# Performance work log

Hardware: AMD Instinct MI355X
Metric: run time of the kernel (lower is better)

## Reference

```python
import jax, jax.numpy as jnp
import numpy as np

EPS = 1e-08

def setup_inputs() -> dict:
    key = jax.random.key(0)
    k1, k2, k3, k4 = jax.random.split(key, 4)
    b, n, in_c, out_c, style_dim = 8, 4096, 512, 512, 512
    x = jax.random.normal(k1, (b, n, in_c), dtype=jnp.float32)
    style = jax.random.normal(k2, (b, style_dim), dtype=jnp.float32)
    # kaiming-ish scaled weights
    weight = jax.random.normal(k3, (1, in_c, out_c), dtype=jnp.float32) * np.float32(np.sqrt(2.0 / (1 + 0.2**2) / in_c))
    mod_w = jax.random.normal(k4, (in_c, style_dim), dtype=jnp.float32) * np.float32(np.sqrt(2.0 / (1 + 0.2**2) / style_dim))
    mod_b = jnp.zeros((in_c,), dtype=jnp.float32)
    return {"x": x, "style": style, "weight": weight, "mod_w": mod_w, "mod_b": mod_b}

def reference(x, style, weight, mod_w, mod_b):
    # style fc: (b, style_dim) -> (b, in_c)
    s = style @ mod_w.T + mod_b                      # (b, in)
    # modulate: broadcast base weight (1, in, out) by (s + 1)
    w = weight * (s[:, :, None] + 1.0)               # (b, in, out)
    # demodulate: rsqrt of sum of squares over in dim
    demod = jax.lax.rsqrt(jnp.sum(w * w, axis=1) + EPS)  # (b, out)
    w = w * demod[:, None, :]                        # (b, in, out)
    # batched matmul: (b, n, in) @ (b, in, out) -> (b, n, out)
    out = jnp.einsum('bni,bio->bno', x, w)
    return out
```

## Files before the change

kernel.cpp:

```cpp
#include <hip/hip_runtime.h>
#include <hip/hip_bf16.h>

typedef __bf16 bf16x4 __attribute__((ext_vector_type(4)));
typedef __bf16 bf16x8 __attribute__((ext_vector_type(8)));
typedef float f32x4 __attribute__((ext_vector_type(4)));

#define B_    8
#define NTOK  4096
#define CIN   512
#define COUT  512
#define SDIM  512
#define EPSF  1e-8f

__global__ __launch_bounds__(256) void k_stylefc(
    const float* __restrict__ style, const float* __restrict__ mod_w,
    const float* __restrict__ mod_b, float* __restrict__ m_out) {
  int gw   = (blockIdx.x * 256 + threadIdx.x) >> 6;
  int lane = threadIdx.x & 63;
  int b = gw >> 9;
  int i = gw & 511;
  const float* srow = style + (size_t)b * SDIM;
  const float* wrow = mod_w + (size_t)i * SDIM;
  float acc = 0.f;
#pragma unroll
  for (int k = 0; k < SDIM; k += 64) acc += srow[k + lane] * wrow[k + lane];
#pragma unroll
  for (int off = 32; off; off >>= 1) acc += __shfl_xor(acc, off, 64);
  if (lane == 0) m_out[b * CIN + i] = acc + mod_b[i] + 1.0f;
}

__global__ __launch_bounds__(256) void k_wprep(
    const float* __restrict__ weight, const float* __restrict__ m_buf,
    __bf16* __restrict__ wT, float* __restrict__ demod) {
  int o = blockIdx.x;
  int tid = threadIdx.x;
  int wid = tid >> 6, lane = tid & 63;
  float acc[B_] = {0.f, 0.f, 0.f, 0.f, 0.f, 0.f, 0.f, 0.f};
#pragma unroll
  for (int rep = 0; rep < 2; ++rep) {
    int i = tid + rep * 256;
    float w = weight[(size_t)i * COUT + o];
    wT[(size_t)o * CIN + i] = (__bf16)w;
#pragma unroll
    for (int b = 0; b < B_; ++b) {
      float wm = w * m_buf[b * CIN + i];
      acc[b] += wm * wm;
    }
  }
  __shared__ float red[4][B_];
#pragma unroll
  for (int b = 0; b < B_; ++b) {
    float v = acc[b];
#pragma unroll
    for (int off = 32; off; off >>= 1) v += __shfl_xor(v, off, 64);
    if (lane == 0) red[wid][b] = v;
  }
  __syncthreads();
  if (tid < B_) {
    float s = red[0][tid] + red[1][tid] + red[2][tid] + red[3][tid];
    demod[tid * COUT + o] = rsqrtf(s + EPSF);
  }
}

__global__ __launch_bounds__(256, 2) void k_gemm(
    const float* __restrict__ x, const __bf16* __restrict__ wT,
    const float* __restrict__ m_buf, const float* __restrict__ demod,
    float* __restrict__ out) {
  int bid  = blockIdx.x;
  int xcd  = bid & 7;
  int slot = bid >> 3;
  int panel = xcd * 32 + (slot >> 2);
  int nb   = slot & 3;
  int b    = panel >> 5;
  int mb   = panel & 31;

  __shared__ uint4 lds_u4[1024];
  char* lds = (char*)lds_u4;

  int tid  = threadIdx.x;
  int wid  = tid >> 6, lane = tid & 63;
  int wr   = wid >> 1, wc = wid & 1;

  f32x4 acc[4][4] = {};

  const float*  xbase = x + ((size_t)b * NTOK + (size_t)mb * 128) * CIN;
  const float*  mrow  = m_buf + b * CIN;

  int arow = tid >> 3, aseg = tid & 7;
  int brow = tid >> 2, bchk = tid & 3;

  for (int k0 = 0; k0 < CIN; k0 += 32) {
    float4 mv = *(const float4*)(mrow + k0 + aseg * 4);
#pragma unroll
    for (int p = 0; p < 4; ++p) {
      int r = arow + p * 32;
      float4 xv = *(const float4*)(xbase + (size_t)r * CIN + k0 + aseg * 4);
      bf16x4 hv;
      hv[0] = (__bf16)(xv.x * mv.x);
      hv[1] = (__bf16)(xv.y * mv.y);
      hv[2] = (__bf16)(xv.z * mv.z);
      hv[3] = (__bf16)(xv.w * mv.w);
      int chunk = aseg >> 1;
      int sw = chunk ^ ((r >> 1) & 3);
      *(bf16x4*)(lds + r * 64 + sw * 16 + (aseg & 1) * 8) = hv;
    }
#pragma unroll
    for (int p = 0; p < 2; ++p) {
      int r = brow + p * 64;
      int o = nb * 128 + r;
      uint4 v = *(const uint4*)(wT + (size_t)o * CIN + k0 + bchk * 8);
      int sw = bchk ^ ((r >> 1) & 3);
      *(uint4*)(lds + 8192 + r * 64 + sw * 16) = v;
    }
    __syncthreads();

    bf16x8 af[4], bfr[4];
#pragma unroll
    for (int mm = 0; mm < 4; ++mm) {
      int r = wr * 64 + mm * 16 + (lane & 15);
      int sw = (lane >> 4) ^ ((r >> 1) & 3);
      af[mm] = *(const bf16x8*)(lds + r * 64 + sw * 16);
    }
#pragma unroll
    for (int nn = 0; nn < 4; ++nn) {
      int r = wc * 64 + nn * 16 + (lane & 15);
      int sw = (lane >> 4) ^ ((r >> 1) & 3);
      bfr[nn] = *(const bf16x8*)(lds + 8192 + r * 64 + sw * 16);
    }
#pragma unroll
    for (int mm = 0; mm < 4; ++mm)
#pragma unroll
      for (int nn = 0; nn < 4; ++nn)
        acc[mm][nn] = __builtin_amdgcn_mfma_f32_16x16x32_bf16(
            af[mm], bfr[nn], acc[mm][nn], 0, 0, 0);
    __syncthreads();
  }

  float* obase = out + ((size_t)b * NTOK + (size_t)mb * 128) * COUT + nb * 128;
  const float* drow = demod + b * COUT + nb * 128;
#pragma unroll
  for (int nn = 0; nn < 4; ++nn) {
    int col = wc * 64 + nn * 16 + (lane & 15);
    float d = drow[col];
#pragma unroll
    for (int mm = 0; mm < 4; ++mm) {
      int r0 = wr * 64 + mm * 16 + (lane >> 4) * 4;
#pragma unroll
      for (int j = 0; j < 4; ++j)
        obase[(size_t)(r0 + j) * COUT + col] = acc[mm][nn][j] * d;
    }
  }
}

extern "C" void kernel_launch(void* const* d_in, const int* in_sizes, int n_in,
                              void* d_out, int out_size, void* d_ws, size_t ws_size,
                              hipStream_t stream) {
  const float* x      = (const float*)d_in[0];
  const float* style  = (const float*)d_in[1];
  const float* weight = (const float*)d_in[2];
  const float* mod_w  = (const float*)d_in[3];
  const float* mod_b  = (const float*)d_in[4];
  float* out = (float*)d_out;

  float*  m_buf = (float*)d_ws;
  float*  demod = m_buf + B_ * CIN;
  __bf16* wT    = (__bf16*)((char*)d_ws + 2 * B_ * CIN * sizeof(float));

  k_stylefc<<<dim3((B_ * CIN) / 4), dim3(256), 0, stream>>>(style, mod_w, mod_b, m_buf);
  k_wprep<<<dim3(COUT), dim3(256), 0, stream>>>(weight, m_buf, wT, demod);
  k_gemm<<<dim3(8 * 32 * 4), dim3(256), 0, stream>>>(x, wT, m_buf, demod, out);
}
```

Baseline: 46.77 us.

## Double-buffer GEMM tiles with async global-to-LDS loads for weights

The GEMM main loop now uses two LDS buffers per operand. The next k-step's x tile is prefetched into registers and the weight tile is issued with global_load_lds direct-to-LDS copies, both overlapping the MFMA work on the current buffer, which leaves one barrier per step. The B tile drops its swizzle and the launch bounds rise to 4 blocks per CU. In exchange, LDS use doubles to 32KB and register pressure grows from the prefetched x values under a tighter occupancy bound. The B reads are unswizzled and may hit LDS bank conflicts, and the async copy relies on the following barrier for completion.

```diff
diff --git a/kernel.cpp b/kernel.cpp
--- a/kernel.cpp
+++ b/kernel.cpp
@@ -62,7 +62,13 @@
   }
 }
 
-__global__ __launch_bounds__(256, 2) void k_gemm(
+__device__ __forceinline__ void async_copy16(void* lds_dst, const void* gsrc) {
+  __builtin_amdgcn_global_load_lds(
+      (const __attribute__((address_space(1))) unsigned int*)gsrc,
+      (__attribute__((address_space(3))) unsigned int*)lds_dst, 16, 0, 0);
+}
+
+__global__ __launch_bounds__(256, 4) void k_gemm(
     const float* __restrict__ x, const __bf16* __restrict__ wT,
     const float* __restrict__ m_buf, const float* __restrict__ demod,
     float* __restrict__ out) {
@@ -74,8 +80,12 @@
   int b    = panel >> 5;
   int mb   = panel & 31;
 
-  __shared__ uint4 lds_u4[1024];
+  __shared__ uint4 lds_u4[2048];
   char* lds = (char*)lds_u4;
+  char* Ab0 = lds;
+  char* Ab1 = lds + 8192;
+  char* Bb0 = lds + 16384;
+  char* Bb1 = lds + 24576;
 
   int tid  = threadIdx.x;
   int wid  = tid >> 6, lane = tid & 63;
@@ -85,47 +95,52 @@
 
   const float*  xbase = x + ((size_t)b * NTOK + (size_t)mb * 128) * CIN;
   const float*  mrow  = m_buf + b * CIN;
+  const __bf16* wTb   = wT + (size_t)(nb * 128) * CIN;
 
   int arow = tid >> 3, aseg = tid & 7;
-  int brow = tid >> 2, bchk = tid & 3;
-
-  for (int k0 = 0; k0 < CIN; k0 += 32) {
-    float4 mv = *(const float4*)(mrow + k0 + aseg * 4);
+
+  float4 xa[4];
+  float4 mv;
+
+  auto loadA = [&](int k0) {
+    mv = *(const float4*)(mrow + k0 + aseg * 4);
+#pragma unroll
+    for (int p = 0; p < 4; ++p)
+      xa[p] = *(const float4*)(xbase + (size_t)(arow + p * 32) * CIN + k0 + aseg * 4);
+  };
+  auto writeA = [&](char* Ab) {
 #pragma unroll
     for (int p = 0; p < 4; ++p) {
       int r = arow + p * 32;
-      float4 xv = *(const float4*)(xbase + (size_t)r * CIN + k0 + aseg * 4);
       bf16x4 hv;
-      hv[0] = (__bf16)(xv.x * mv.x);
-      hv[1] = (__bf16)(xv.y * mv.y);
-      hv[2] = (__bf16)(xv.z * mv.z);
-      hv[3] = (__bf16)(xv.w * mv.w);
-      int chunk = aseg >> 1;
-      int sw = chunk ^ ((r >> 1) & 3);
-      *(bf16x4*)(lds + r * 64 + sw * 16 + (aseg & 1) * 8) = hv;
-    }
-#pragma unroll
-    for (int p = 0; p < 2; ++p) {
-      int r = brow + p * 64;
-      int o = nb * 128 + r;
-      uint4 v = *(const uint4*)(wT + (size_t)o * CIN + k0 + bchk * 8);
-      int sw = bchk ^ ((r >> 1) & 3);
-      *(uint4*)(lds + 8192 + r * 64 + sw * 16) = v;
-    }
-    __syncthreads();
-
+      hv[0] = (__bf16)(xa[p].x * mv.x);
+      hv[1] = (__bf16)(xa[p].y * mv.y);
+      hv[2] = (__bf16)(xa[p].z * mv.z);
+      hv[3] = (__bf16)(xa[p].w * mv.w);
+      int sw = (aseg >> 1) ^ ((r >> 1) & 3);
+      *(bf16x4*)(Ab + r * 64 + sw * 16 + (aseg & 1) * 8) = hv;
+    }
+  };
+  auto issueB = [&](int k0, char* Bb) {
+#pragma unroll
+    for (int inst = 0; inst < 2; ++inst) {
+      int row = wid * 32 + inst * 16 + (lane >> 2);
+      const char* g = (const char*)(wTb + (size_t)row * CIN + k0) + (lane & 3) * 16;
+      async_copy16(Bb + wid * 2048 + inst * 1024, g);
+    }
+  };
+  auto mmaStep = [&](const char* Ab, const char* Bb) {
     bf16x8 af[4], bfr[4];
 #pragma unroll
     for (int mm = 0; mm < 4; ++mm) {
       int r = wr * 64 + mm * 16 + (lane & 15);
       int sw = (lane >> 4) ^ ((r >> 1) & 3);
-      af[mm] = *(const bf16x8*)(lds + r * 64 + sw * 16);
+      af[mm] = *(const bf16x8*)(Ab + r * 64 + sw * 16);
     }
 #pragma unroll
     for (int nn = 0; nn < 4; ++nn) {
       int r = wc * 64 + nn * 16 + (lane & 15);
-      int sw = (lane >> 4) ^ ((r >> 1) & 3);
-      bfr[nn] = *(const bf16x8*)(lds + 8192 + r * 64 + sw * 16);
+      bfr[nn] = *(const bf16x8*)(Bb + r * 64 + (lane >> 4) * 16);
     }
 #pragma unroll
     for (int mm = 0; mm < 4; ++mm)
@@ -133,8 +148,28 @@
       for (int nn = 0; nn < 4; ++nn)
         acc[mm][nn] = __builtin_amdgcn_mfma_f32_16x16x32_bf16(
             af[mm], bfr[nn], acc[mm][nn], 0, 0, 0);
+  };
+
+  loadA(0);
+  issueB(0, Bb0);
+  writeA(Ab0);
+  __syncthreads();
+
+#pragma unroll
+  for (int ks = 0; ks < 15; ++ks) {
+    const bool cur0 = ((ks & 1) == 0);
+    char* Ac = cur0 ? Ab0 : Ab1;
+    char* Bc = cur0 ? Bb0 : Bb1;
+    char* An = cur0 ? Ab1 : Ab0;
+    char* Bn = cur0 ? Bb1 : Bb0;
+    int k0n = (ks + 1) * 32;
+    issueB(k0n, Bn);
+    loadA(k0n);
+    mmaStep(Ac, Bc);
+    writeA(An);
     __syncthreads();
   }
+  mmaStep(Ab1, Bb1);
 
   float* obase = out + ((size_t)b * NTOK + (size_t)mb * 128) * COUT + nb * 128;
   const float* drow = demod + b * COUT + nb * 128;
```

Result: slower. 59.87 us (+28.0%).

## Restructure GEMM: full-N tiles, pre-swizzled weight image with async LDS double buffer

Applied to the files above, without the earlier changes.

The weight prep kernel now writes the transposed bf16 weight directly in the swizzled LDS tile layout. The GEMM gives each 512-thread block 64 tokens by all 512 output channels, so x is read once per row instead of four times across N-blocks. Weight tiles are streamed into double-buffered LDS with global_load_lds async copies. Activations are loaded straight from global memory into MFMA B-fragments without staging in LDS, and outputs are stored as float4. The trade-off is 64KB of LDS per block, fewer blocks (512), lower occupancy, and uncoalesced-ish direct x fragment loads.

```diff
diff --git a/kernel.cpp b/kernel.cpp
--- a/kernel.cpp
+++ b/kernel.cpp
@@ -1,7 +1,6 @@
 #include <hip/hip_runtime.h>
 #include <hip/hip_bf16.h>
 
-typedef __bf16 bf16x4 __attribute__((ext_vector_type(4)));
 typedef __bf16 bf16x8 __attribute__((ext_vector_type(8)));
 typedef float f32x4 __attribute__((ext_vector_type(4)));
 
@@ -31,19 +30,22 @@
 
 __global__ __launch_bounds__(256) void k_wprep(
     const float* __restrict__ weight, const float* __restrict__ m_buf,
-    __bf16* __restrict__ wT, float* __restrict__ demod) {
+    __bf16* __restrict__ wimg, float* __restrict__ demod) {
   int o = blockIdx.x;
   int tid = threadIdx.x;
   int wid = tid >> 6, lane = tid & 63;
   float acc[B_] = {0.f, 0.f, 0.f, 0.f, 0.f, 0.f, 0.f, 0.f};
 #pragma unroll
   for (int rep = 0; rep < 2; ++rep) {
-    int i = tid + rep * 256;
-    float w = weight[(size_t)i * COUT + o];
-    wT[(size_t)o * CIN + i] = (__bf16)w;
+    int k = tid + rep * 256;
+    float w = weight[(size_t)k * COUT + o];
+    int kt = k >> 5, kl = k & 31, s = kl >> 3, ko = kl & 7;
+    int sl = s ^ ((o >> 1) & 3);
+    *(__bf16*)((char*)wimg + (size_t)kt * 32768 + o * 64 + sl * 16 + ko * 2) =
+        (__bf16)w;
 #pragma unroll
     for (int b = 0; b < B_; ++b) {
-      float wm = w * m_buf[b * CIN + i];
+      float wm = w * m_buf[b * CIN + k];
       acc[b] += wm * wm;
     }
   }
@@ -62,92 +64,97 @@
   }
 }
 
-__global__ __launch_bounds__(256, 2) void k_gemm(
-    const float* __restrict__ x, const __bf16* __restrict__ wT,
+__device__ __forceinline__ void async_copy16(void* lds_dst, const void* gsrc) {
+  __builtin_amdgcn_global_load_lds(
+      (const __attribute__((address_space(1))) unsigned int*)gsrc,
+      (__attribute__((address_space(3))) unsigned int*)lds_dst, 16, 0, 0);
+}
+
+__global__ __launch_bounds__(512) void k_gemm(
+    const float* __restrict__ x, const __bf16* __restrict__ wimg,
     const float* __restrict__ m_buf, const float* __restrict__ demod,
     float* __restrict__ out) {
-  int bid  = blockIdx.x;
-  int xcd  = bid & 7;
-  int slot = bid >> 3;
-  int panel = xcd * 32 + (slot >> 2);
-  int nb   = slot & 3;
-  int b    = panel >> 5;
-  int mb   = panel & 31;
+  int bid = blockIdx.x;
+  int b   = bid >> 6;
+  int tb  = bid & 63;
 
-  __shared__ uint4 lds_u4[1024];
-  char* lds = (char*)lds_u4;
+  __shared__ uint4 lds_u4[4096];
+  char* W0 = (char*)lds_u4;
+  char* W1 = (char*)lds_u4 + 32768;
 
   int tid  = threadIdx.x;
   int wid  = tid >> 6, lane = tid & 63;
-  int wr   = wid >> 1, wc = wid & 1;
+  int ln15 = lane & 15, s = lane >> 4;
 
   f32x4 acc[4][4] = {};
 
-  const float*  xbase = x + ((size_t)b * NTOK + (size_t)mb * 128) * CIN;
-  const float*  mrow  = m_buf + b * CIN;
+  const float* xb   = x + (size_t)(b * NTOK + tb * 64) * CIN;
+  const float* mrow = m_buf + b * CIN;
+  const char*  isrc = (const char*)wimg;
 
-  int arow = tid >> 3, aseg = tid & 7;
-  int brow = tid >> 2, bchk = tid & 3;
+  auto issueW = [&](int kt, char* Wb) {
+    const char* src = isrc + (size_t)kt * 32768;
+#pragma unroll
+    for (int q = 0; q < 4; ++q) {
+      int off = (q * 8 + wid) * 1024;
+      async_copy16(Wb + off, src + off + lane * 16);
+    }
+  };
 
-  for (int k0 = 0; k0 < CIN; k0 += 32) {
-    float4 mv = *(const float4*)(mrow + k0 + aseg * 4);
+  issueW(0, W0);
+  __syncthreads();
+
 #pragma unroll
-    for (int p = 0; p < 4; ++p) {
-      int r = arow + p * 32;
-      float4 xv = *(const float4*)(xbase + (size_t)r * CIN + k0 + aseg * 4);
-      bf16x4 hv;
-      hv[0] = (__bf16)(xv.x * mv.x);
-      hv[1] = (__bf16)(xv.y * mv.y);
-      hv[2] = (__bf16)(xv.z * mv.z);
-      hv[3] = (__bf16)(xv.w * mv.w);
-      int chunk = aseg >> 1;
-      int sw = chunk ^ ((r >> 1) & 3);
-      *(bf16x4*)(lds + r * 64 + sw * 16 + (aseg & 1) * 8) = hv;
-    }
-#pragma unroll
-    for (int p = 0; p < 2; ++p) {
-      int r = brow + p * 64;
-      int o = nb * 128 + r;
-      uint4 v = *(const uint4*)(wT + (size_t)o * CIN + k0 + bchk * 8);
-      int sw = bchk ^ ((r >> 1) & 3);
-      *(uint4*)(lds + 8192 + r * 64 + sw * 16) = v;
-    }
-    __syncthreads();
-
-    bf16x8 af[4], bfr[4];
+  for (int kt = 0; kt < 16; ++kt) {
+    char* Wc = (kt & 1) ? W1 : W0;
+    char* Wn = (kt & 1) ? W0 : W1;
+    bf16x8 wf[4];
 #pragma unroll
     for (int mm = 0; mm < 4; ++mm) {
-      int r = wr * 64 + mm * 16 + (lane & 15);
-      int sw = (lane >> 4) ^ ((r >> 1) & 3);
-      af[mm] = *(const bf16x8*)(lds + r * 64 + sw * 16);
+      int r = wid * 64 + mm * 16 + ln15;
+      wf[mm] = *(const bf16x8*)(Wc + r * 64 + ((s ^ ((r >> 1) & 3)) << 4));
     }
+    if (kt < 15) issueW(kt + 1, Wn);
+
+    const float* mk = mrow + kt * 32 + s * 8;
+    float4 mv0 = *(const float4*)mk;
+    float4 mv1 = *(const float4*)(mk + 4);
 #pragma unroll
     for (int nn = 0; nn < 4; ++nn) {
-      int r = wc * 64 + nn * 16 + (lane & 15);
-      int sw = (lane >> 4) ^ ((r >> 1) & 3);
-      bfr[nn] = *(const bf16x8*)(lds + 8192 + r * 64 + sw * 16);
+      const float* px = xb + (size_t)(nn * 16 + ln15) * CIN + kt * 32 + s * 8;
+      float4 a0 = *(const float4*)px;
+      float4 a1 = *(const float4*)(px + 4);
+      bf16x8 xf;
+      xf[0] = (__bf16)(a0.x * mv0.x);
+      xf[1] = (__bf16)(a0.y * mv0.y);
+      xf[2] = (__bf16)(a0.z * mv0.z);
+      xf[3] = (__bf16)(a0.w * mv0.w);
+      xf[4] = (__bf16)(a1.x * mv1.x);
+      xf[5] = (__bf16)(a1.y * mv1.y);
+      xf[6] = (__bf16)(a1.z * mv1.z);
+      xf[7] = (__bf16)(a1.w * mv1.w);
+#pragma unroll
+      for (int mm = 0; mm < 4; ++mm)
+        acc[mm][nn] = __builtin_amdgcn_mfma_f32_16x16x32_bf16(
+            wf[mm], xf, acc[mm][nn], 0, 0, 0);
     }
-#pragma unroll
-    for (int mm = 0; mm < 4; ++mm)
-#pragma unroll
-      for (int nn = 0; nn < 4; ++nn)
-        acc[mm][nn] = __builtin_amdgcn_mfma_f32_16x16x32_bf16(
-            af[mm], bfr[nn], acc[mm][nn], 0, 0, 0);
-    __syncthreads();
+    if (kt < 15) __syncthreads();
   }
 
-  float* obase = out + ((size_t)b * NTOK + (size_t)mb * 128) * COUT + nb * 128;
-  const float* drow = demod + b * COUT + nb * 128;
+  float* ob = out + (size_t)(b * NTOK + tb * 64) * COUT;
 #pragma unroll
-  for (int nn = 0; nn < 4; ++nn) {
-    int col = wc * 64 + nn * 16 + (lane & 15);
-    float d = drow[col];
+  for (int mm = 0; mm < 4; ++mm) {
+    int o = wid * 64 + mm * 16 + s * 4;
+    float4 dv = *(const float4*)(demod + b * COUT + o);
 #pragma unroll
-    for (int mm = 0; mm < 4; ++mm) {
-      int r0 = wr * 64 + mm * 16 + (lane >> 4) * 4;
-#pragma unroll
-      for (int j = 0; j < 4; ++j)
-        obase[(size_t)(r0 + j) * COUT + col] = acc[mm][nn][j] * d;
+    for (int nn = 0; nn < 4; ++nn) {
+      int t = nn * 16 + ln15;
+      f32x4 r;
+      r[0] = acc[mm][nn][0] * dv.x;
+      r[1] = acc[mm][nn][1] * dv.y;
+      r[2] = acc[mm][nn][2] * dv.z;
+      r[3] = acc[mm][nn][3] * dv.w;
+      *(f32x4*)(ob + (size_t)t * COUT + o) = r;
     }
   }
 }
@@ -164,9 +171,9 @@
 
   float*  m_buf = (float*)d_ws;
   float*  demod = m_buf + B_ * CIN;
-  __bf16* wT    = (__bf16*)((char*)d_ws + 2 * B_ * CIN * sizeof(float));
+  __bf16* wimg  = (__bf16*)((char*)d_ws + 2 * B_ * CIN * sizeof(float));
 
   k_stylefc<<<dim3((B_ * CIN) / 4), dim3(256), 0, stream>>>(style, mod_w, mod_b, m_buf);
-  k_wprep<<<dim3(COUT), dim3(256), 0, stream>>>(weight, m_buf, wT, demod);
-  k_gemm<<<dim3(8 * 32 * 4), dim3(256), 0, stream>>>(x, wT, m_buf, demod, out);
+  k_wprep<<<dim3(COUT), dim3(256), 0, stream>>>(weight, m_buf, wimg, demod);
+  k_gemm<<<dim3(8 * 64), dim3(512), 0, stream>>>(x, wimg, m_buf, demod, out);
 }
```

Result: slower. 108.8 us (+132.6%).
